# Kernel tuning notes

Measured on AMD Instinct MI355X. Metric: run time of the kernel, lower is better.

The kernel has to match this reference:

```python
import jax, jax.numpy as jnp
import numpy as np

N, E, IN, HID, H, C = 10000, 320000, 64, 64, 4, 64
HC = H * C  # 256


def setup_inputs() -> dict:
    key = jax.random.key(0)
    ks = jax.random.split(key, 40)
    ki = iter(range(40))
    def nrm(shape, scale=0.05):
        return jax.random.normal(ks[next(ki)], shape, dtype=jnp.float32) * scale
    inp = {
        "x": jax.random.normal(ks[next(ki)], (N, IN), dtype=jnp.float32),
        "edge_index": jax.random.randint(ks[next(ki)], (2, E), 0, N, dtype=jnp.int64),
        "lin_w": nrm((IN, HID)), "lin_b": nrm((HID,)),
    }
    dims_in = [HID, HC, HC]
    for i, di in enumerate(dims_in):
        inp[f"gat_w{i}"] = nrm((di, HC))
        inp[f"att_src{i}"] = nrm((H, C))
        inp[f"att_dst{i}"] = nrm((H, C))
        inp[f"gat_b{i}"] = nrm((HC,))
        inp[f"ln_g{i}"] = jnp.ones((HC,), jnp.float32)
        inp[f"ln_b{i}"] = jnp.zeros((HC,), jnp.float32)
    inp["ffn_w1"] = nrm((HC, 2 * HID)); inp["ffn_b1"] = nrm((2 * HID,))
    inp["ffn_w2"] = nrm((2 * HID, 64)); inp["ffn_b2"] = nrm((64,))
    return inp


def _layernorm(x, g, b, eps=1e-5):
    m = jnp.mean(x, -1, keepdims=True)
    v = jnp.var(x, -1, keepdims=True)
    return (x - m) * jax.lax.rsqrt(v + eps) * g + b


def _gat(x, src, dst, w, a_src, a_dst, b):
    # PyG GATConv: per-head linear, additive attention, segment softmax over dst
    xl = (x @ w).reshape(-1, H, C)              # [N,H,C]
    e = jax.nn.leaky_relu(jnp.sum(xl * a_src, -1)[src]
                          + jnp.sum(xl * a_dst, -1)[dst], 0.2)  # [E,H]
    emax = jax.ops.segment_max(e, dst, num_segments=N)
    ex = jnp.exp(e - emax[dst])
    alpha = ex / jax.ops.segment_sum(ex, dst, num_segments=N)[dst]
    out = jax.ops.segment_sum(xl[src] * alpha[:, :, None], dst, num_segments=N)
    return out.reshape(-1, HC) + b


def reference(x, edge_index, lin_w, lin_b,
              gat_w0, att_src0, att_dst0, gat_b0, ln_g0, ln_b0,
              gat_w1, att_src1, att_dst1, gat_b1, ln_g1, ln_b1,
              gat_w2, att_src2, att_dst2, gat_b2, ln_g2, ln_b2,
              ffn_w1, ffn_b1, ffn_w2, ffn_b2):
    loops = jnp.arange(N, dtype=edge_index.dtype)
    src = jnp.concatenate([edge_index[0], loops])  # add_self_loops=True
    dst = jnp.concatenate([edge_index[1], loops])
    h = jax.nn.relu(x @ lin_w + lin_b)
    layers = [(gat_w0, att_src0, att_dst0, gat_b0, ln_g0, ln_b0),
              (gat_w1, att_src1, att_dst1, gat_b1, ln_g1, ln_b1),
              (gat_w2, att_src2, att_dst2, gat_b2, ln_g2, ln_b2)]
    for (w, a_s, a_d, b, g, lb) in layers:
        residual = h
        h = jax.nn.elu(_gat(h, src, dst, w, a_s, a_d, b))
        if residual.shape[-1] != h.shape[-1]:
            residual = jnp.pad(residual, ((0, 0), (0, h.shape[-1] - residual.shape[-1])))
        h = _layernorm(h + residual, g, lb)  # dropout is identity in eval mode
    h = jax.nn.relu(h @ ffn_w1 + ffn_b1)
    return h @ ffn_w2 + ffn_b2
```

## Files before the change

### kernel.cpp

```cpp
#include <hip/hip_runtime.h>

#define N_NODES 10000
#define N_EDGES 320000
#define EL (N_EDGES + N_NODES)
#define HC 256
#define CAP 96

using bf16x8 = __attribute__((ext_vector_type(8))) short;
using f32x4  = __attribute__((ext_vector_type(4))) float;

__device__ __forceinline__ float bf2f(unsigned short u) {
  union { unsigned int i; float f; } v; v.i = ((unsigned int)u) << 16; return v.f;
}
__device__ __forceinline__ unsigned short f2bf(float f) {
  union { float f; unsigned int i; } v; v.f = f;
  unsigned int r = (v.i + 0x7FFFu + ((v.i >> 16) & 1u)) >> 16;
  return (unsigned short)r;
}


__device__ __forceinline__ void convw_body(const float* __restrict__ w,
                                           unsigned short* __restrict__ bt,
                                           int K, int idx) {
  int half = K >> 1;
  if (idx >= 256 * half) return;
  int col = idx / half;
  int k2 = (idx % half) * 2;
  ushort2 o;
  o.x = f2bf(w[(size_t)k2 * 256 + col]);
  o.y = f2bf(w[(size_t)(k2 + 1) * 256 + col]);
  *(ushort2*)(bt + (size_t)col * K + k2) = o;
}

__global__ __launch_bounds__(256) void prep_kernel(
    int* __restrict__ cnt,
    const float* __restrict__ w0, unsigned short* __restrict__ bt0,
    const float* __restrict__ w1, unsigned short* __restrict__ bt1,
    const float* __restrict__ w2, unsigned short* __restrict__ bt2) {
  int b = blockIdx.x, tid = threadIdx.x;
  if (b < 40) {
    int i = b * 256 + tid;
    if (i < N_NODES) cnt[i] = 0;
  } else if (b < 72) {
    convw_body(w0, bt0, 64, (b - 40) * 256 + tid);
  } else if (b < 200) {
    convw_body(w1, bt1, 256, (b - 72) * 256 + tid);
  } else {
    convw_body(w2, bt2, 256, (b - 200) * 256 + tid);
  }
}


__global__ __launch_bounds__(256) void scatter_lin_kernel(
    const int* __restrict__ edges, int* __restrict__ cnt, int* __restrict__ slots,
    const float* __restrict__ A, const float* __restrict__ B,
    const float* __restrict__ bias, float* __restrict__ C) {
  int tid = threadIdx.x;
  if (blockIdx.x < 1290) {
    int e = blockIdx.x * 256 + tid;
    if (e >= EL) return;
    int s, d;
    if (e < N_EDGES) { s = edges[e]; d = edges[N_EDGES + e]; }
    else { s = d = e - N_EDGES; }
    int pos = atomicAdd(&cnt[d], 1);
    slots[d * CAP + pos] = s;
    return;
  }
  __shared__ float As[16][36];
  __shared__ float Bs[32][64];
  int row0 = (blockIdx.x - 1290) * 16;
  int g = tid >> 6, lane = tid & 63;
  float acc[4];
#pragma unroll
  for (int r = 0; r < 4; ++r) acc[r] = 0.f;
  for (int k0 = 0; k0 < 64; k0 += 32) {
    if (tid < 128) {
      int r = tid >> 3;
      int kc = (tid & 7) << 2;
      *(float4*)&As[r][kc] = *(const float4*)(A + (size_t)(row0 + r) * 64 + k0 + kc);
    }
    {
#pragma unroll
      for (int i = 0; i < 2; ++i) {
        int fidx = (i * 256 + tid) * 4;
        int kk = fidx >> 6;
        int cc = fidx & 63;
        *(float4*)&Bs[kk][cc] = *(const float4*)(B + (size_t)(k0 + kk) * 64 + cc);
      }
    }
    __syncthreads();
#pragma unroll
    for (int kk = 0; kk < 32; kk += 4) {
      float a4[4][4];
#pragma unroll
      for (int rr = 0; rr < 4; ++rr) {
        float4 t = *(const float4*)&As[g * 4 + rr][kk];
        a4[rr][0] = t.x; a4[rr][1] = t.y; a4[rr][2] = t.z; a4[rr][3] = t.w;
      }
#pragma unroll
      for (int u = 0; u < 4; ++u) {
        float b = Bs[kk + u][lane];
#pragma unroll
        for (int rr = 0; rr < 4; ++rr) acc[rr] = fmaf(a4[rr][u], b, acc[rr]);
      }
    }
    __syncthreads();
  }
#pragma unroll
  for (int rr = 0; rr < 4; ++rr) {
    int row = row0 + g * 4 + rr;
    C[(size_t)row * 64 + lane] = fmaxf(acc[rr] + bias[lane], 0.f);
  }
}


template <int K>
__global__ __launch_bounds__(256) void gemm_attn_mfma(
    const float* __restrict__ A, const unsigned short* __restrict__ Bt,
    unsigned short* __restrict__ Cb,
    const float* __restrict__ att_src, const float* __restrict__ att_dst,
    float* __restrict__ asrc_out, float* __restrict__ adst_out) {
  __shared__ __align__(16) unsigned short Asw[16 * 64];
  __shared__ __align__(16) unsigned short Bsw[256 * 64];
  int tid = threadIdx.x;
  int wave = tid >> 6, lane = tid & 63;
  int r = lane & 15, g = lane >> 4;
  int row0 = blockIdx.x * 16;

  f32x4 acc[4];
#pragma unroll
  for (int i = 0; i < 4; ++i) acc[i] = {0.f, 0.f, 0.f, 0.f};

  for (int k0 = 0; k0 < K; k0 += 64) {
    {
      int ar = tid >> 4;
      int kc = (tid & 15) << 2;
      float4 av = *(const float4*)(A + (size_t)(row0 + ar) * K + k0 + kc);
      ushort4 o;
      o.x = f2bf(av.x); o.y = f2bf(av.y); o.z = f2bf(av.z); o.w = f2bf(av.w);
      *(ushort4*)((char*)Asw + ((ar * 128 + kc * 2) ^ ((ar & 7) << 4))) = o;
    }
#pragma unroll
    for (int i = 0; i < 8; ++i) {
      int idx = i * 256 + tid;
      int col = idx >> 3;
      int kc8 = idx & 7;
      uint4 v = *(const uint4*)(Bt + (size_t)col * K + k0 + kc8 * 8);
      *(uint4*)((char*)Bsw + ((col * 128 + kc8 * 16) ^ ((col & 7) << 4))) = v;
    }
    __syncthreads();
#pragma unroll
    for (int chunk = 0; chunk < 2; ++chunk) {
      bf16x8 af = *(const bf16x8*)((char*)Asw +
                    ((r * 128 + chunk * 64 + g * 16) ^ ((r & 7) << 4)));
#pragma unroll
      for (int i = 0; i < 4; ++i) {
        int col = (wave * 4 + i) * 16 + r;
        bf16x8 bfr = *(const bf16x8*)((char*)Bsw +
                       ((col * 128 + chunk * 64 + g * 16) ^ ((col & 7) << 4)));
        acc[i] = __builtin_amdgcn_mfma_f32_16x16x32_bf16(af, bfr, acc[i], 0, 0, 0);
      }
    }
    __syncthreads();
  }

  float asv[4], adv[4];
#pragma unroll
  for (int i = 0; i < 4; ++i) {
    int col = (wave * 4 + i) * 16 + r;
    asv[i] = att_src[col];
    adv[i] = att_dst[col];
  }
#pragma unroll
  for (int j = 0; j < 4; ++j) {
    float ps = acc[0][j] * asv[0] + acc[1][j] * asv[1] + acc[2][j] * asv[2] + acc[3][j] * asv[3];
    float pd = acc[0][j] * adv[0] + acc[1][j] * adv[1] + acc[2][j] * adv[2] + acc[3][j] * adv[3];
#pragma unroll
    for (int m = 8; m >= 1; m >>= 1) {
      ps += __shfl_xor(ps, m);
      pd += __shfl_xor(pd, m);
    }
    if (r == 0) {
      int row = row0 + g * 4 + j;
      asrc_out[row * 4 + wave] = ps;
      adst_out[row * 4 + wave] = pd;
    }
  }

#pragma unroll
  for (int i = 0; i < 4; ++i) {
    int col = (wave * 4 + i) * 16 + r;
#pragma unroll
    for (int j = 0; j < 4; ++j) {
      int row = row0 + g * 4 + j;
      Cb[(size_t)row * 256 + col] = f2bf(acc[i][j]);
    }
  }
}


template <int MODE>
__global__ __launch_bounds__(256) void agg_kernel(
    const int* __restrict__ cnt, const int* __restrict__ slots,
    const float* __restrict__ asrc, const float* __restrict__ adst,
    const unsigned short* __restrict__ xb, const float* __restrict__ bias,
    const float* __restrict__ resid, const float* __restrict__ ln_g,
    const float* __restrict__ ln_b, float* __restrict__ hout) {
  int w = threadIdx.x >> 6, lane = threadIdx.x & 63;
  int n = blockIdx.x * 4 + w;
  int lh = lane & 31;
  int half = lane >> 5;
  int h = lh >> 3;
  int ch8 = lh << 3;
  float ad = adst[n * 4 + h];

  int i0 = n * CAP;
  int deg = cnt[n];
  int len0 = (deg + 1) >> 1;
  int beg = i0 + (half ? len0 : 0);
  int end = i0 + (half ? deg : len0);
  int last = end - 1;

  float a0 = 0.f, a1 = 0.f, a2 = 0.f, a3 = 0.f, a4 = 0.f, a5 = 0.f, a6 = 0.f, a7 = 0.f;
  float wsum = 0.f;

  int sA[4];
#pragma unroll
  for (int j = 0; j < 4; ++j) sA[j] = slots[min(beg + j, last)];
  float ca[4]; uint4 cx[4];
#pragma unroll
  for (int j = 0; j < 4; ++j) {
    ca[j] = asrc[sA[j] * 4 + h];
    cx[j] = *(const uint4*)(xb + (size_t)sA[j] * HC + ch8);
  }
#pragma unroll
  for (int j = 0; j < 4; ++j) sA[j] = slots[min(beg + 4 + j, last)];

  for (int base = beg; base < end; base += 4) {
    float na[4]; uint4 nx[4];
#pragma unroll
    for (int j = 0; j < 4; ++j) {
      na[j] = asrc[sA[j] * 4 + h];
      nx[j] = *(const uint4*)(xb + (size_t)sA[j] * HC + ch8);
    }
#pragma unroll
    for (int j = 0; j < 4; ++j) sA[j] = slots[min(base + 8 + j, last)];
#pragma unroll
    for (int j = 0; j < 4; ++j) {
      float e = ca[j] + ad;
      e = e > 0.f ? e : 0.2f * e;
      float wg = __expf(e);
      wg = (base + j < end) ? wg : 0.f;
      wsum += wg;
      a0 = fmaf(wg, bf2f((unsigned short)(cx[j].x & 0xffff)), a0);
      a1 = fmaf(wg, bf2f((unsigned short)(cx[j].x >> 16)), a1);
      a2 = fmaf(wg, bf2f((unsigned short)(cx[j].y & 0xffff)), a2);
      a3 = fmaf(wg, bf2f((unsigned short)(cx[j].y >> 16)), a3);
      a4 = fmaf(wg, bf2f((unsigned short)(cx[j].z & 0xffff)), a4);
      a5 = fmaf(wg, bf2f((unsigned short)(cx[j].z >> 16)), a5);
      a6 = fmaf(wg, bf2f((unsigned short)(cx[j].w & 0xffff)), a6);
      a7 = fmaf(wg, bf2f((unsigned short)(cx[j].w >> 16)), a7);
    }
#pragma unroll
    for (int j = 0; j < 4; ++j) { ca[j] = na[j]; cx[j] = nx[j]; }
  }

  a0 += __shfl_xor(a0, 32); a1 += __shfl_xor(a1, 32);
  a2 += __shfl_xor(a2, 32); a3 += __shfl_xor(a3, 32);
  a4 += __shfl_xor(a4, 32); a5 += __shfl_xor(a5, 32);
  a6 += __shfl_xor(a6, 32); a7 += __shfl_xor(a7, 32);
  wsum += __shfl_xor(wsum, 32);

  int cb = ch8 + half * 4;
  float v0 = half ? a4 : a0;
  float v1 = half ? a5 : a1;
  float v2 = half ? a6 : a2;
  float v3 = half ? a7 : a3;

  float rw = 1.f / wsum;
  float4 b4 = *(const float4*)(bias + cb);
  v0 = fmaf(v0, rw, b4.x);
  v1 = fmaf(v1, rw, b4.y);
  v2 = fmaf(v2, rw, b4.z);
  v3 = fmaf(v3, rw, b4.w);
  v0 = v0 > 0.f ? v0 : __expf(v0) - 1.f;
  v1 = v1 > 0.f ? v1 : __expf(v1) - 1.f;
  v2 = v2 > 0.f ? v2 : __expf(v2) - 1.f;
  v3 = v3 > 0.f ? v3 : __expf(v3) - 1.f;

  if constexpr (MODE == 0) {
    if (cb < 64) {
      float4 r = *(const float4*)(resid + (size_t)n * 64 + cb);
      v0 += r.x; v1 += r.y; v2 += r.z; v3 += r.w;
    }
  } else {
    float4 r = *(const float4*)(resid + (size_t)n * HC + cb);
    v0 += r.x; v1 += r.y; v2 += r.z; v3 += r.w;
  }

  float s1 = v0 + v1 + v2 + v3;
  float s2 = v0 * v0 + v1 * v1 + v2 * v2 + v3 * v3;
#pragma unroll
  for (int m = 32; m >= 1; m >>= 1) {
    s1 += __shfl_xor(s1, m);
    s2 += __shfl_xor(s2, m);
  }
  float mean = s1 * (1.f / 256.f);
  float var = s2 * (1.f / 256.f) - mean * mean;
  float inv = rsqrtf(var + 1e-5f);

  float4 g4 = *(const float4*)(ln_g + cb);
  float4 lb4 = *(const float4*)(ln_b + cb);
  float4 o;
  o.x = (v0 - mean) * inv * g4.x + lb4.x;
  o.y = (v1 - mean) * inv * g4.y + lb4.y;
  o.z = (v2 - mean) * inv * g4.z + lb4.z;
  o.w = (v3 - mean) * inv * g4.w + lb4.w;
  *(float4*)(hout + (size_t)n * HC + cb) = o;
}


__global__ __launch_bounds__(256) void ffn_kernel(const float* __restrict__ A,
                                                  const float* __restrict__ w1,
                                                  const float* __restrict__ b1,
                                                  const float* __restrict__ w2,
                                                  const float* __restrict__ b2,
                                                  float* __restrict__ out) {
  __shared__ float As[16][36];
  __shared__ float Bs[32][128];
  __shared__ float Ms[16][132];
  int tid = threadIdx.x;
  int row0 = blockIdx.x * 16;
  int g = tid >> 6, lane = tid & 63;

  {
    int colBase = lane * 2;
    float acc[4][2];
#pragma unroll
    for (int r = 0; r < 4; ++r) { acc[r][0] = 0.f; acc[r][1] = 0.f; }
    for (int k0 = 0; k0 < 256; k0 += 32) {
      if (tid < 128) {
        int r = tid >> 3;
        int kc = (tid & 7) << 2;
        *(float4*)&As[r][kc] = *(const float4*)(A + (size_t)(row0 + r) * 256 + k0 + kc);
      }
#pragma unroll
      for (int i = 0; i < 4; ++i) {
        int fidx = (i * 256 + tid) * 4;
        int kk = fidx >> 7;
        int cc = fidx & 127;
        *(float4*)&Bs[kk][cc] = *(const float4*)(w1 + (size_t)(k0 + kk) * 128 + cc);
      }
      __syncthreads();
#pragma unroll
      for (int kk = 0; kk < 32; kk += 4) {
        float a4[4][4];
#pragma unroll
        for (int rr = 0; rr < 4; ++rr) {
          float4 t = *(const float4*)&As[g * 4 + rr][kk];
          a4[rr][0] = t.x; a4[rr][1] = t.y; a4[rr][2] = t.z; a4[rr][3] = t.w;
        }
#pragma unroll
        for (int u = 0; u < 4; ++u) {
          float2 b = *(const float2*)&Bs[kk + u][colBase];
#pragma unroll
          for (int rr = 0; rr < 4; ++rr) {
            acc[rr][0] = fmaf(a4[rr][u], b.x, acc[rr][0]);
            acc[rr][1] = fmaf(a4[rr][u], b.y, acc[rr][1]);
          }
        }
      }
      __syncthreads();
    }
    float bb0 = b1[colBase], bb1 = b1[colBase + 1];
#pragma unroll
    for (int rr = 0; rr < 4; ++rr) {
      Ms[g * 4 + rr][colBase]     = fmaxf(acc[rr][0] + bb0, 0.f);
      Ms[g * 4 + rr][colBase + 1] = fmaxf(acc[rr][1] + bb1, 0.f);
    }
  }
  __syncthreads();

  {
    float acc[4];
#pragma unroll
    for (int r = 0; r < 4; ++r) acc[r] = 0.f;
    for (int k0 = 0; k0 < 128; k0 += 32) {
#pragma unroll
      for (int i = 0; i < 2; ++i) {
        int fidx = (i * 256 + tid) * 4;
        int kk = fidx >> 6;
        int cc = fidx & 63;
        *(float4*)&Bs[kk][cc] = *(const float4*)(w2 + (size_t)(k0 + kk) * 64 + cc);
      }
      __syncthreads();
#pragma unroll
      for (int kk = 0; kk < 32; ++kk) {
        float b = Bs[kk][lane];
#pragma unroll
        for (int rr = 0; rr < 4; ++rr)
          acc[rr] = fmaf(Ms[g * 4 + rr][k0 + kk], b, acc[rr]);
      }
      __syncthreads();
    }
    float bb = b2[lane];
#pragma unroll
    for (int rr = 0; rr < 4; ++rr) {
      int row = row0 + g * 4 + rr;
      out[(size_t)row * 64 + lane] = acc[rr] + bb;
    }
  }
}


extern "C" void kernel_launch(void* const* d_in, const int* in_sizes, int n_in,
                              void* d_out, int out_size, void* d_ws, size_t ws_size,
                              hipStream_t stream) {
  (void)in_sizes; (void)n_in; (void)out_size; (void)ws_size;
  const float* x      = (const float*)d_in[0];
  const int*   edges  = (const int*)d_in[1];
  const float* lin_w  = (const float*)d_in[2];
  const float* lin_b  = (const float*)d_in[3];
  const float* gat_w[3] = {(const float*)d_in[4], (const float*)d_in[10], (const float*)d_in[16]};
  const float* att_s[3] = {(const float*)d_in[5], (const float*)d_in[11], (const float*)d_in[17]};
  const float* att_d[3] = {(const float*)d_in[6], (const float*)d_in[12], (const float*)d_in[18]};
  const float* gat_b[3] = {(const float*)d_in[7], (const float*)d_in[13], (const float*)d_in[19]};
  const float* ln_g[3]  = {(const float*)d_in[8], (const float*)d_in[14], (const float*)d_in[20]};
  const float* ln_b[3]  = {(const float*)d_in[9], (const float*)d_in[15], (const float*)d_in[21]};
  const float* ffn_w1 = (const float*)d_in[22];
  const float* ffn_b1 = (const float*)d_in[23];
  const float* ffn_w2 = (const float*)d_in[24];
  const float* ffn_b2 = (const float*)d_in[25];

  char* p = (char*)d_ws;
  auto alloc = [&](size_t bytes) {
    char* q = p;
    p += (bytes + 255) & ~(size_t)255;
    return q;
  };
  int* cnt   = (int*)alloc(N_NODES * 4);
  int* slots = (int*)alloc((size_t)N_NODES * CAP * 4);
  float* h0  = (float*)alloc((size_t)N_NODES * 64 * 4);
  float* hA  = (float*)alloc((size_t)N_NODES * HC * 4);
  float* hB  = (float*)alloc((size_t)N_NODES * HC * 4);
  unsigned short* xb = (unsigned short*)alloc((size_t)N_NODES * HC * 2);
  float* as4 = (float*)alloc((size_t)N_NODES * 16);
  float* ad4 = (float*)alloc((size_t)N_NODES * 16);
  unsigned short* bt0 = (unsigned short*)alloc(256 * 64 * 2);
  unsigned short* bt1 = (unsigned short*)alloc(256 * 256 * 2);
  unsigned short* bt2 = (unsigned short*)alloc(256 * 256 * 2);

  const int gblk = N_NODES / 16;
  const int nblk = N_NODES / 4;

  prep_kernel<<<328, 256, 0, stream>>>(cnt, gat_w[0], bt0, gat_w[1], bt1, gat_w[2], bt2);
  scatter_lin_kernel<<<1290 + 625, 256, 0, stream>>>(edges, cnt, slots, x, lin_w, lin_b, h0);

  gemm_attn_mfma<64><<<gblk, 256, 0, stream>>>(h0, bt0, xb, att_s[0], att_d[0], as4, ad4);
  agg_kernel<0><<<nblk, 256, 0, stream>>>(cnt, slots, as4, ad4, xb, gat_b[0], h0,
                                          ln_g[0], ln_b[0], hA);
  gemm_attn_mfma<256><<<gblk, 256, 0, stream>>>(hA, bt1, xb, att_s[1], att_d[1], as4, ad4);
  agg_kernel<1><<<nblk, 256, 0, stream>>>(cnt, slots, as4, ad4, xb, gat_b[1], hA,
                                          ln_g[1], ln_b[1], hB);
  gemm_attn_mfma<256><<<gblk, 256, 0, stream>>>(hB, bt2, xb, att_s[2], att_d[2], as4, ad4);
  agg_kernel<1><<<nblk, 256, 0, stream>>>(cnt, slots, as4, ad4, xb, gat_b[2], hB,
                                          ln_g[2], ln_b[2], hA);

  ffn_kernel<<<gblk, 256, 0, stream>>>(hA, ffn_w1, ffn_b1, ffn_w2, ffn_b2, (float*)d_out);
}
```

Before: 153.9 us.

## Fuse all stages into one cooperative persistent kernel with grid syncs

Replaces the nine separate kernel launches with a single cooperative persistent kernel. Each former kernel becomes a grid-stride phase, and the phases are separated by grid.sync(). The aim is to remove launch overhead and the drain/refill gaps between kernels. In exchange, the shared-memory union limits occupancy, each grid barrier has its own cost, and the grid size is set from an occupancy query that assumes 256 CUs.

```diff
diff --git a/kernel.cpp b/kernel.cpp
--- a/kernel.cpp
+++ b/kernel.cpp
@@ -1,4 +1,7 @@
 #include <hip/hip_runtime.h>
+#include <hip/hip_cooperative_groups.h>
+
+namespace cg = cooperative_groups;
 
 #define N_NODES 10000
 #define N_EDGES 320000
@@ -18,12 +21,25 @@
   return (unsigned short)r;
 }
 
+struct MegaParams {
+  const int* edges;
+  const float* x; const float* lin_w; const float* lin_b;
+  const float* gw0; const float* as0; const float* ad0; const float* gb0; const float* lg0; const float* lb0;
+  const float* gw1; const float* as1; const float* ad1; const float* gb1; const float* lg1; const float* lb1;
+  const float* gw2; const float* as2; const float* ad2; const float* gb2; const float* lg2; const float* lb2;
+  const float* fw1; const float* fb1; const float* fw2; const float* fb2;
+  int* cnt; int* slots;
+  float* h0; float* hA; float* hB;
+  unsigned short* xb;
+  float* as4; float* ad4;
+  unsigned short* bt0; unsigned short* bt1; unsigned short* bt2;
+  float* out;
+};
 
 __device__ __forceinline__ void convw_body(const float* __restrict__ w,
                                            unsigned short* __restrict__ bt,
                                            int K, int idx) {
   int half = K >> 1;
-  if (idx >= 256 * half) return;
   int col = idx / half;
   int k2 = (idx % half) * 2;
   ushort2 o;
@@ -32,61 +48,25 @@
   *(ushort2*)(bt + (size_t)col * K + k2) = o;
 }
 
-__global__ __launch_bounds__(256) void prep_kernel(
-    int* __restrict__ cnt,
-    const float* __restrict__ w0, unsigned short* __restrict__ bt0,
-    const float* __restrict__ w1, unsigned short* __restrict__ bt1,
-    const float* __restrict__ w2, unsigned short* __restrict__ bt2) {
-  int b = blockIdx.x, tid = threadIdx.x;
-  if (b < 40) {
-    int i = b * 256 + tid;
-    if (i < N_NODES) cnt[i] = 0;
-  } else if (b < 72) {
-    convw_body(w0, bt0, 64, (b - 40) * 256 + tid);
-  } else if (b < 200) {
-    convw_body(w1, bt1, 256, (b - 72) * 256 + tid);
-  } else {
-    convw_body(w2, bt2, 256, (b - 200) * 256 + tid);
-  }
-}
-
-
-__global__ __launch_bounds__(256) void scatter_lin_kernel(
-    const int* __restrict__ edges, int* __restrict__ cnt, int* __restrict__ slots,
-    const float* __restrict__ A, const float* __restrict__ B,
-    const float* __restrict__ bias, float* __restrict__ C) {
-  int tid = threadIdx.x;
-  if (blockIdx.x < 1290) {
-    int e = blockIdx.x * 256 + tid;
-    if (e >= EL) return;
-    int s, d;
-    if (e < N_EDGES) { s = edges[e]; d = edges[N_EDGES + e]; }
-    else { s = d = e - N_EDGES; }
-    int pos = atomicAdd(&cnt[d], 1);
-    slots[d * CAP + pos] = s;
-    return;
-  }
-  __shared__ float As[16][36];
-  __shared__ float Bs[32][64];
-  int row0 = (blockIdx.x - 1290) * 16;
+__device__ void lin_tile(char* smem, int t, const float* __restrict__ A,
+                         const float* __restrict__ B, const float* __restrict__ bias,
+                         float* __restrict__ C, int tid) {
+  float (*As)[36] = (float(*)[36])smem;
+  float (*Bs)[64] = (float(*)[64])(smem + 2304);
+  int row0 = t * 16;
   int g = tid >> 6, lane = tid & 63;
-  float acc[4];
-#pragma unroll
-  for (int r = 0; r < 4; ++r) acc[r] = 0.f;
+  float acc[4] = {0.f, 0.f, 0.f, 0.f};
   for (int k0 = 0; k0 < 64; k0 += 32) {
     if (tid < 128) {
       int r = tid >> 3;
       int kc = (tid & 7) << 2;
       *(float4*)&As[r][kc] = *(const float4*)(A + (size_t)(row0 + r) * 64 + k0 + kc);
     }
-    {
-#pragma unroll
-      for (int i = 0; i < 2; ++i) {
-        int fidx = (i * 256 + tid) * 4;
-        int kk = fidx >> 6;
-        int cc = fidx & 63;
-        *(float4*)&Bs[kk][cc] = *(const float4*)(B + (size_t)(k0 + kk) * 64 + cc);
-      }
+#pragma unroll
+    for (int i = 0; i < 2; ++i) {
+      int fidx = (i * 256 + tid) * 4;
+      *(float4*)&Bs[fidx >> 6][fidx & 63] =
+          *(const float4*)(B + (size_t)(k0 + (fidx >> 6)) * 64 + (fidx & 63));
     }
     __syncthreads();
 #pragma unroll
@@ -94,8 +74,8 @@
       float a4[4][4];
 #pragma unroll
       for (int rr = 0; rr < 4; ++rr) {
-        float4 t = *(const float4*)&As[g * 4 + rr][kk];
-        a4[rr][0] = t.x; a4[rr][1] = t.y; a4[rr][2] = t.z; a4[rr][3] = t.w;
+        float4 tv = *(const float4*)&As[g * 4 + rr][kk];
+        a4[rr][0] = tv.x; a4[rr][1] = tv.y; a4[rr][2] = tv.z; a4[rr][3] = tv.w;
       }
 #pragma unroll
       for (int u = 0; u < 4; ++u) {
@@ -113,19 +93,17 @@
   }
 }
 
-
 template <int K>
-__global__ __launch_bounds__(256) void gemm_attn_mfma(
-    const float* __restrict__ A, const unsigned short* __restrict__ Bt,
-    unsigned short* __restrict__ Cb,
-    const float* __restrict__ att_src, const float* __restrict__ att_dst,
-    float* __restrict__ asrc_out, float* __restrict__ adst_out) {
-  __shared__ __align__(16) unsigned short Asw[16 * 64];
-  __shared__ __align__(16) unsigned short Bsw[256 * 64];
-  int tid = threadIdx.x;
+__device__ void mfma_tile(char* smem, int t, const float* __restrict__ A,
+                          const unsigned short* __restrict__ Bt,
+                          unsigned short* __restrict__ Cb,
+                          const float* __restrict__ att_src, const float* __restrict__ att_dst,
+                          float* __restrict__ asrc_out, float* __restrict__ adst_out, int tid) {
+  char* Asw = smem;
+  char* Bsw = smem + 2048;
   int wave = tid >> 6, lane = tid & 63;
   int r = lane & 15, g = lane >> 4;
-  int row0 = blockIdx.x * 16;
+  int row0 = t * 16;
 
   f32x4 acc[4];
 #pragma unroll
@@ -138,7 +116,7 @@
       float4 av = *(const float4*)(A + (size_t)(row0 + ar) * K + k0 + kc);
       ushort4 o;
       o.x = f2bf(av.x); o.y = f2bf(av.y); o.z = f2bf(av.z); o.w = f2bf(av.w);
-      *(ushort4*)((char*)Asw + ((ar * 128 + kc * 2) ^ ((ar & 7) << 4))) = o;
+      *(ushort4*)(Asw + ((ar * 128 + kc * 2) ^ ((ar & 7) << 4))) = o;
     }
 #pragma unroll
     for (int i = 0; i < 8; ++i) {
@@ -146,18 +124,16 @@
       int col = idx >> 3;
       int kc8 = idx & 7;
       uint4 v = *(const uint4*)(Bt + (size_t)col * K + k0 + kc8 * 8);
-      *(uint4*)((char*)Bsw + ((col * 128 + kc8 * 16) ^ ((col & 7) << 4))) = v;
+      *(uint4*)(Bsw + ((col * 128 + kc8 * 16) ^ ((col & 7) << 4))) = v;
     }
     __syncthreads();
 #pragma unroll
     for (int chunk = 0; chunk < 2; ++chunk) {
-      bf16x8 af = *(const bf16x8*)((char*)Asw +
-                    ((r * 128 + chunk * 64 + g * 16) ^ ((r & 7) << 4)));
+      bf16x8 af = *(const bf16x8*)(Asw + ((r * 128 + chunk * 64 + g * 16) ^ ((r & 7) << 4)));
 #pragma unroll
       for (int i = 0; i < 4; ++i) {
         int col = (wave * 4 + i) * 16 + r;
-        bf16x8 bfr = *(const bf16x8*)((char*)Bsw +
-                       ((col * 128 + chunk * 64 + g * 16) ^ ((col & 7) << 4)));
+        bf16x8 bfr = *(const bf16x8*)(Bsw + ((col * 128 + chunk * 64 + g * 16) ^ ((col & 7) << 4)));
         acc[i] = __builtin_amdgcn_mfma_f32_16x16x32_bf16(af, bfr, acc[i], 0, 0, 0);
       }
     }
@@ -198,16 +174,14 @@
   }
 }
 
-
 template <int MODE>
-__global__ __launch_bounds__(256) void agg_kernel(
-    const int* __restrict__ cnt, const int* __restrict__ slots,
-    const float* __restrict__ asrc, const float* __restrict__ adst,
-    const unsigned short* __restrict__ xb, const float* __restrict__ bias,
-    const float* __restrict__ resid, const float* __restrict__ ln_g,
-    const float* __restrict__ ln_b, float* __restrict__ hout) {
-  int w = threadIdx.x >> 6, lane = threadIdx.x & 63;
-  int n = blockIdx.x * 4 + w;
+__device__ void agg_group(int gidx, const int* __restrict__ cnt, const int* __restrict__ slots,
+                          const float* __restrict__ asrc, const float* __restrict__ adst,
+                          const unsigned short* __restrict__ xb, const float* __restrict__ bias,
+                          const float* __restrict__ resid, const float* __restrict__ ln_g,
+                          const float* __restrict__ ln_b, float* __restrict__ hout, int tid) {
+  int w = tid >> 6, lane = tid & 63;
+  int n = gidx * 4 + w;
   int lh = lane & 31;
   int half = lane >> 5;
   int h = lh >> 3;
@@ -319,18 +293,14 @@
   *(float4*)(hout + (size_t)n * HC + cb) = o;
 }
 
-
-__global__ __launch_bounds__(256) void ffn_kernel(const float* __restrict__ A,
-                                                  const float* __restrict__ w1,
-                                                  const float* __restrict__ b1,
-                                                  const float* __restrict__ w2,
-                                                  const float* __restrict__ b2,
-                                                  float* __restrict__ out) {
-  __shared__ float As[16][36];
-  __shared__ float Bs[32][128];
-  __shared__ float Ms[16][132];
-  int tid = threadIdx.x;
-  int row0 = blockIdx.x * 16;
+__device__ void ffn_tile(char* smem, int t, const float* __restrict__ A,
+                         const float* __restrict__ w1, const float* __restrict__ b1,
+                         const float* __restrict__ w2, const float* __restrict__ b2,
+                         float* __restrict__ out, int tid) {
+  float (*As)[36] = (float(*)[36])smem;
+  float (*Bs)[128] = (float(*)[128])(smem + 2304);
+  float (*Ms)[132] = (float(*)[132])(smem + 18688);
+  int row0 = t * 16;
   int g = tid >> 6, lane = tid & 63;
 
   {
@@ -347,9 +317,8 @@
 #pragma unroll
       for (int i = 0; i < 4; ++i) {
         int fidx = (i * 256 + tid) * 4;
-        int kk = fidx >> 7;
-        int cc = fidx & 127;
-        *(float4*)&Bs[kk][cc] = *(const float4*)(w1 + (size_t)(k0 + kk) * 128 + cc);
+        *(float4*)&Bs[fidx >> 7][fidx & 127] =
+            *(const float4*)(w1 + (size_t)(k0 + (fidx >> 7)) * 128 + (fidx & 127));
       }
       __syncthreads();
 #pragma unroll
@@ -357,8 +326,8 @@
         float a4[4][4];
 #pragma unroll
         for (int rr = 0; rr < 4; ++rr) {
-          float4 t = *(const float4*)&As[g * 4 + rr][kk];
-          a4[rr][0] = t.x; a4[rr][1] = t.y; a4[rr][2] = t.z; a4[rr][3] = t.w;
+          float4 tv = *(const float4*)&As[g * 4 + rr][kk];
+          a4[rr][0] = tv.x; a4[rr][1] = tv.y; a4[rr][2] = tv.z; a4[rr][3] = tv.w;
         }
 #pragma unroll
         for (int u = 0; u < 4; ++u) {
@@ -382,16 +351,13 @@
   __syncthreads();
 
   {
-    float acc[4];
-#pragma unroll
-    for (int r = 0; r < 4; ++r) acc[r] = 0.f;
+    float acc[4] = {0.f, 0.f, 0.f, 0.f};
     for (int k0 = 0; k0 < 128; k0 += 32) {
 #pragma unroll
       for (int i = 0; i < 2; ++i) {
         int fidx = (i * 256 + tid) * 4;
-        int kk = fidx >> 6;
-        int cc = fidx & 63;
-        *(float4*)&Bs[kk][cc] = *(const float4*)(w2 + (size_t)(k0 + kk) * 64 + cc);
+        *(float4*)&Bs[fidx >> 6][fidx & 63] =
+            *(const float4*)(w2 + (size_t)(k0 + (fidx >> 6)) * 64 + (fidx & 63));
       }
       __syncthreads();
 #pragma unroll
@@ -410,6 +376,56 @@
       out[(size_t)row * 64 + lane] = acc[rr] + bb;
     }
   }
+}
+
+
+__global__ __launch_bounds__(256) void mega_kernel(MegaParams p) {
+  __shared__ __align__(16) char smem[34816];
+  cg::grid_group grid = cg::this_grid();
+  int tid = threadIdx.x;
+  int gtid = blockIdx.x * 256 + tid;
+  int stride = gridDim.x * 256;
+
+  for (int i = gtid; i < N_NODES; i += stride) p.cnt[i] = 0;
+  for (int i = gtid; i < 256 * 32; i += stride) convw_body(p.gw0, p.bt0, 64, i);
+  for (int i = gtid; i < 256 * 128; i += stride) convw_body(p.gw1, p.bt1, 256, i);
+  for (int i = gtid; i < 256 * 128; i += stride) convw_body(p.gw2, p.bt2, 256, i);
+  grid.sync();
+
+  for (int t = blockIdx.x; t < 625; t += gridDim.x)
+    lin_tile(smem, t, p.x, p.lin_w, p.lin_b, p.h0, tid);
+  for (int e = gtid; e < EL; e += stride) {
+    int s, d;
+    if (e < N_EDGES) { s = p.edges[e]; d = p.edges[N_EDGES + e]; }
+    else { s = d = e - N_EDGES; }
+    int pos = atomicAdd(&p.cnt[d], 1);
+    p.slots[d * CAP + pos] = s;
+  }
+  grid.sync();
+
+  for (int t = blockIdx.x; t < 625; t += gridDim.x)
+    mfma_tile<64>(smem, t, p.h0, p.bt0, p.xb, p.as0, p.ad0, p.as4, p.ad4, tid);
+  grid.sync();
+  for (int g2 = blockIdx.x; g2 < 2500; g2 += gridDim.x)
+    agg_group<0>(g2, p.cnt, p.slots, p.as4, p.ad4, p.xb, p.gb0, p.h0, p.lg0, p.lb0, p.hA, tid);
+  grid.sync();
+
+  for (int t = blockIdx.x; t < 625; t += gridDim.x)
+    mfma_tile<256>(smem, t, p.hA, p.bt1, p.xb, p.as1, p.ad1, p.as4, p.ad4, tid);
+  grid.sync();
+  for (int g2 = blockIdx.x; g2 < 2500; g2 += gridDim.x)
+    agg_group<1>(g2, p.cnt, p.slots, p.as4, p.ad4, p.xb, p.gb1, p.hA, p.lg1, p.lb1, p.hB, tid);
+  grid.sync();
+
+  for (int t = blockIdx.x; t < 625; t += gridDim.x)
+    mfma_tile<256>(smem, t, p.hB, p.bt2, p.xb, p.as2, p.ad2, p.as4, p.ad4, tid);
+  grid.sync();
+  for (int g2 = blockIdx.x; g2 < 2500; g2 += gridDim.x)
+    agg_group<1>(g2, p.cnt, p.slots, p.as4, p.ad4, p.xb, p.gb2, p.hB, p.lg2, p.lb2, p.hA, tid);
+  grid.sync();
+
+  for (int t = blockIdx.x; t < 625; t += gridDim.x)
+    ffn_tile(smem, t, p.hA, p.fw1, p.fb1, p.fw2, p.fb2, p.out, tid);
 }
 
 
@@ -417,25 +433,11 @@
                               void* d_out, int out_size, void* d_ws, size_t ws_size,
                               hipStream_t stream) {
   (void)in_sizes; (void)n_in; (void)out_size; (void)ws_size;
-  const float* x      = (const float*)d_in[0];
-  const int*   edges  = (const int*)d_in[1];
-  const float* lin_w  = (const float*)d_in[2];
-  const float* lin_b  = (const float*)d_in[3];
-  const float* gat_w[3] = {(const float*)d_in[4], (const float*)d_in[10], (const float*)d_in[16]};
-  const float* att_s[3] = {(const float*)d_in[5], (const float*)d_in[11], (const float*)d_in[17]};
-  const float* att_d[3] = {(const float*)d_in[6], (const float*)d_in[12], (const float*)d_in[18]};
-  const float* gat_b[3] = {(const float*)d_in[7], (const float*)d_in[13], (const float*)d_in[19]};
-  const float* ln_g[3]  = {(const float*)d_in[8], (const float*)d_in[14], (const float*)d_in[20]};
-  const float* ln_b[3]  = {(const float*)d_in[9], (const float*)d_in[15], (const float*)d_in[21]};
-  const float* ffn_w1 = (const float*)d_in[22];
-  const float* ffn_b1 = (const float*)d_in[23];
-  const float* ffn_w2 = (const float*)d_in[24];
-  const float* ffn_b2 = (const float*)d_in[25];
-
-  char* p = (char*)d_ws;
+
+  char* wp = (char*)d_ws;
   auto alloc = [&](size_t bytes) {
-    char* q = p;
-    p += (bytes + 255) & ~(size_t)255;
+    char* q = wp;
+    wp += (bytes + 255) & ~(size_t)255;
     return q;
   };
   int* cnt   = (int*)alloc(N_NODES * 4);
@@ -450,21 +452,28 @@
   unsigned short* bt1 = (unsigned short*)alloc(256 * 256 * 2);
   unsigned short* bt2 = (unsigned short*)alloc(256 * 256 * 2);
 
-  const int gblk = N_NODES / 16;
-  const int nblk = N_NODES / 4;
-
-  prep_kernel<<<328, 256, 0, stream>>>(cnt, gat_w[0], bt0, gat_w[1], bt1, gat_w[2], bt2);
-  scatter_lin_kernel<<<1290 + 625, 256, 0, stream>>>(edges, cnt, slots, x, lin_w, lin_b, h0);
-
-  gemm_attn_mfma<64><<<gblk, 256, 0, stream>>>(h0, bt0, xb, att_s[0], att_d[0], as4, ad4);
-  agg_kernel<0><<<nblk, 256, 0, stream>>>(cnt, slots, as4, ad4, xb, gat_b[0], h0,
-                                          ln_g[0], ln_b[0], hA);
-  gemm_attn_mfma<256><<<gblk, 256, 0, stream>>>(hA, bt1, xb, att_s[1], att_d[1], as4, ad4);
-  agg_kernel<1><<<nblk, 256, 0, stream>>>(cnt, slots, as4, ad4, xb, gat_b[1], hA,
-                                          ln_g[1], ln_b[1], hB);
-  gemm_attn_mfma<256><<<gblk, 256, 0, stream>>>(hB, bt2, xb, att_s[2], att_d[2], as4, ad4);
-  agg_kernel<1><<<nblk, 256, 0, stream>>>(cnt, slots, as4, ad4, xb, gat_b[2], hB,
-                                          ln_g[2], ln_b[2], hA);
-
-  ffn_kernel<<<gblk, 256, 0, stream>>>(hA, ffn_w1, ffn_b1, ffn_w2, ffn_b2, (float*)d_out);
-}
+  MegaParams p;
+  p.edges = (const int*)d_in[1];
+  p.x = (const float*)d_in[0]; p.lin_w = (const float*)d_in[2]; p.lin_b = (const float*)d_in[3];
+  p.gw0 = (const float*)d_in[4];  p.as0 = (const float*)d_in[5];  p.ad0 = (const float*)d_in[6];
+  p.gb0 = (const float*)d_in[7];  p.lg0 = (const float*)d_in[8];  p.lb0 = (const float*)d_in[9];
+  p.gw1 = (const float*)d_in[10]; p.as1 = (const float*)d_in[11]; p.ad1 = (const float*)d_in[12];
+  p.gb1 = (const float*)d_in[13]; p.lg1 = (const float*)d_in[14]; p.lb1 = (const float*)d_in[15];
+  p.gw2 = (const float*)d_in[16]; p.as2 = (const float*)d_in[17]; p.ad2 = (const float*)d_in[18];
+  p.gb2 = (const float*)d_in[19]; p.lg2 = (const float*)d_in[20]; p.lb2 = (const float*)d_in[21];
+  p.fw1 = (const float*)d_in[22]; p.fb1 = (const float*)d_in[23];
+  p.fw2 = (const float*)d_in[24]; p.fb2 = (const float*)d_in[25];
+  p.cnt = cnt; p.slots = slots; p.h0 = h0; p.hA = hA; p.hB = hB;
+  p.xb = xb; p.as4 = as4; p.ad4 = ad4; p.bt0 = bt0; p.bt1 = bt1; p.bt2 = bt2;
+  p.out = (float*)d_out;
+
+  int nb = 0;
+  hipOccupancyMaxActiveBlocksPerMultiprocessor(&nb, mega_kernel, 256, 0);
+  if (nb < 1) nb = 1;
+  if (nb > 8) nb = 8;
+  int grid = nb * 256;
+  if (grid > 2500) grid = 2500;
+
+  void* kargs[] = {(void*)&p};
+  hipLaunchCooperativeKernel((void*)mega_kernel, dim3(grid), dim3(256), kargs, 0, stream);
+}
```

Result: slower. 551.3 us (+258.3%).

## Store hidden activations in bf16 and fold weight conversion into scatter kernel

Applied to the files above, without the earlier changes.

Intermediate node features (h0, hA, hB) are now stored as bf16 instead of fp32. The GEMM loads them directly without converting, while the aggregation residual path and the FFN widen them on load. This halves the activation traffic between kernels and removes the per-load f32-to-bf16 conversion in the GEMM. The weight bf16 transposition moves from the prep kernel into extra blocks of the scatter/linear kernel, leaving prep to only zero the counters. The trade-off is lower precision in the residual and LayerNorm outputs.

```diff
diff --git a/kernel.cpp b/kernel.cpp
--- a/kernel.cpp
+++ b/kernel.cpp
@@ -19,11 +19,16 @@
 }
 
 
+__global__ __launch_bounds__(256) void prep_kernel(int* __restrict__ cnt) {
+  int i = blockIdx.x * 256 + threadIdx.x;
+  if (i < N_NODES) cnt[i] = 0;
+}
+
+
 __device__ __forceinline__ void convw_body(const float* __restrict__ w,
                                            unsigned short* __restrict__ bt,
                                            int K, int idx) {
   int half = K >> 1;
-  if (idx >= 256 * half) return;
   int col = idx / half;
   int k2 = (idx % half) * 2;
   ushort2 o;
@@ -32,32 +37,17 @@
   *(ushort2*)(bt + (size_t)col * K + k2) = o;
 }
 
-__global__ __launch_bounds__(256) void prep_kernel(
-    int* __restrict__ cnt,
+__global__ __launch_bounds__(256) void scatter_lin_kernel(
+    const int* __restrict__ edges, int* __restrict__ cnt, int* __restrict__ slots,
+    const float* __restrict__ A, const float* __restrict__ B,
+    const float* __restrict__ bias, unsigned short* __restrict__ C,
     const float* __restrict__ w0, unsigned short* __restrict__ bt0,
     const float* __restrict__ w1, unsigned short* __restrict__ bt1,
     const float* __restrict__ w2, unsigned short* __restrict__ bt2) {
-  int b = blockIdx.x, tid = threadIdx.x;
-  if (b < 40) {
-    int i = b * 256 + tid;
-    if (i < N_NODES) cnt[i] = 0;
-  } else if (b < 72) {
-    convw_body(w0, bt0, 64, (b - 40) * 256 + tid);
-  } else if (b < 200) {
-    convw_body(w1, bt1, 256, (b - 72) * 256 + tid);
-  } else {
-    convw_body(w2, bt2, 256, (b - 200) * 256 + tid);
-  }
-}
-
-
-__global__ __launch_bounds__(256) void scatter_lin_kernel(
-    const int* __restrict__ edges, int* __restrict__ cnt, int* __restrict__ slots,
-    const float* __restrict__ A, const float* __restrict__ B,
-    const float* __restrict__ bias, float* __restrict__ C) {
   int tid = threadIdx.x;
-  if (blockIdx.x < 1290) {
-    int e = blockIdx.x * 256 + tid;
+  int b = blockIdx.x;
+  if (b < 1290) {
+    int e = b * 256 + tid;
     if (e >= EL) return;
     int s, d;
     if (e < N_EDGES) { s = edges[e]; d = edges[N_EDGES + e]; }
@@ -66,27 +56,28 @@
     slots[d * CAP + pos] = s;
     return;
   }
+  if (b >= 1915) {
+    if (b < 1947) convw_body(w0, bt0, 64, (b - 1915) * 256 + tid);
+    else if (b < 2075) convw_body(w1, bt1, 256, (b - 1947) * 256 + tid);
+    else convw_body(w2, bt2, 256, (b - 2075) * 256 + tid);
+    return;
+  }
   __shared__ float As[16][36];
   __shared__ float Bs[32][64];
-  int row0 = (blockIdx.x - 1290) * 16;
+  int row0 = (b - 1290) * 16;
   int g = tid >> 6, lane = tid & 63;
-  float acc[4];
-#pragma unroll
-  for (int r = 0; r < 4; ++r) acc[r] = 0.f;
+  float acc[4] = {0.f, 0.f, 0.f, 0.f};
   for (int k0 = 0; k0 < 64; k0 += 32) {
     if (tid < 128) {
       int r = tid >> 3;
       int kc = (tid & 7) << 2;
       *(float4*)&As[r][kc] = *(const float4*)(A + (size_t)(row0 + r) * 64 + k0 + kc);
     }
-    {
-#pragma unroll
-      for (int i = 0; i < 2; ++i) {
-        int fidx = (i * 256 + tid) * 4;
-        int kk = fidx >> 6;
-        int cc = fidx & 63;
-        *(float4*)&Bs[kk][cc] = *(const float4*)(B + (size_t)(k0 + kk) * 64 + cc);
-      }
+#pragma unroll
+    for (int i = 0; i < 2; ++i) {
+      int fidx = (i * 256 + tid) * 4;
+      *(float4*)&Bs[fidx >> 6][fidx & 63] =
+          *(const float4*)(B + (size_t)(k0 + (fidx >> 6)) * 64 + (fidx & 63));
     }
     __syncthreads();
 #pragma unroll
@@ -99,9 +90,9 @@
       }
 #pragma unroll
       for (int u = 0; u < 4; ++u) {
-        float b = Bs[kk + u][lane];
-#pragma unroll
-        for (int rr = 0; rr < 4; ++rr) acc[rr] = fmaf(a4[rr][u], b, acc[rr]);
+        float bb = Bs[kk + u][lane];
+#pragma unroll
+        for (int rr = 0; rr < 4; ++rr) acc[rr] = fmaf(a4[rr][u], bb, acc[rr]);
       }
     }
     __syncthreads();
@@ -109,14 +100,14 @@
 #pragma unroll
   for (int rr = 0; rr < 4; ++rr) {
     int row = row0 + g * 4 + rr;
-    C[(size_t)row * 64 + lane] = fmaxf(acc[rr] + bias[lane], 0.f);
+    C[(size_t)row * 64 + lane] = f2bf(fmaxf(acc[rr] + bias[lane], 0.f));
   }
 }
 
 
 template <int K>
 __global__ __launch_bounds__(256) void gemm_attn_mfma(
-    const float* __restrict__ A, const unsigned short* __restrict__ Bt,
+    const unsigned short* __restrict__ A, const unsigned short* __restrict__ Bt,
     unsigned short* __restrict__ Cb,
     const float* __restrict__ att_src, const float* __restrict__ att_dst,
     float* __restrict__ asrc_out, float* __restrict__ adst_out) {
@@ -135,10 +126,8 @@
     {
       int ar = tid >> 4;
       int kc = (tid & 15) << 2;
-      float4 av = *(const float4*)(A + (size_t)(row0 + ar) * K + k0 + kc);
-      ushort4 o;
-      o.x = f2bf(av.x); o.y = f2bf(av.y); o.z = f2bf(av.z); o.w = f2bf(av.w);
-      *(ushort4*)((char*)Asw + ((ar * 128 + kc * 2) ^ ((ar & 7) << 4))) = o;
+      ushort4 av = *(const ushort4*)(A + (size_t)(row0 + ar) * K + k0 + kc);
+      *(ushort4*)((char*)Asw + ((ar * 128 + kc * 2) ^ ((ar & 7) << 4))) = av;
     }
 #pragma unroll
     for (int i = 0; i < 8; ++i) {
@@ -204,8 +193,8 @@
     const int* __restrict__ cnt, const int* __restrict__ slots,
     const float* __restrict__ asrc, const float* __restrict__ adst,
     const unsigned short* __restrict__ xb, const float* __restrict__ bias,
-    const float* __restrict__ resid, const float* __restrict__ ln_g,
-    const float* __restrict__ ln_b, float* __restrict__ hout) {
+    const unsigned short* __restrict__ resid, const float* __restrict__ ln_g,
+    const float* __restrict__ ln_b, unsigned short* __restrict__ hout) {
   int w = threadIdx.x >> 6, lane = threadIdx.x & 63;
   int n = blockIdx.x * 4 + w;
   int lh = lane & 31;
@@ -290,12 +279,12 @@
 
   if constexpr (MODE == 0) {
     if (cb < 64) {
-      float4 r = *(const float4*)(resid + (size_t)n * 64 + cb);
-      v0 += r.x; v1 += r.y; v2 += r.z; v3 += r.w;
+      ushort4 r4 = *(const ushort4*)(resid + (size_t)n * 64 + cb);
+      v0 += bf2f(r4.x); v1 += bf2f(r4.y); v2 += bf2f(r4.z); v3 += bf2f(r4.w);
     }
   } else {
-    float4 r = *(const float4*)(resid + (size_t)n * HC + cb);
-    v0 += r.x; v1 += r.y; v2 += r.z; v3 += r.w;
+    ushort4 r4 = *(const ushort4*)(resid + (size_t)n * HC + cb);
+    v0 += bf2f(r4.x); v1 += bf2f(r4.y); v2 += bf2f(r4.z); v3 += bf2f(r4.w);
   }
 
   float s1 = v0 + v1 + v2 + v3;
@@ -311,16 +300,16 @@
 
   float4 g4 = *(const float4*)(ln_g + cb);
   float4 lb4 = *(const float4*)(ln_b + cb);
-  float4 o;
-  o.x = (v0 - mean) * inv * g4.x + lb4.x;
-  o.y = (v1 - mean) * inv * g4.y + lb4.y;
-  o.z = (v2 - mean) * inv * g4.z + lb4.z;
-  o.w = (v3 - mean) * inv * g4.w + lb4.w;
-  *(float4*)(hout + (size_t)n * HC + cb) = o;
-}
-
-
-__global__ __launch_bounds__(256) void ffn_kernel(const float* __restrict__ A,
+  ushort4 o;
+  o.x = f2bf((v0 - mean) * inv * g4.x + lb4.x);
+  o.y = f2bf((v1 - mean) * inv * g4.y + lb4.y);
+  o.z = f2bf((v2 - mean) * inv * g4.z + lb4.z);
+  o.w = f2bf((v3 - mean) * inv * g4.w + lb4.w);
+  *(ushort4*)(hout + (size_t)n * HC + cb) = o;
+}
+
+
+__global__ __launch_bounds__(256) void ffn_kernel(const unsigned short* __restrict__ A,
                                                   const float* __restrict__ w1,
                                                   const float* __restrict__ b1,
                                                   const float* __restrict__ w2,
@@ -342,14 +331,17 @@
       if (tid < 128) {
         int r = tid >> 3;
         int kc = (tid & 7) << 2;
-        *(float4*)&As[r][kc] = *(const float4*)(A + (size_t)(row0 + r) * 256 + k0 + kc);
+        ushort4 av = *(const ushort4*)(A + (size_t)(row0 + r) * 256 + k0 + kc);
+        As[r][kc]     = bf2f(av.x);
+        As[r][kc + 1] = bf2f(av.y);
+        As[r][kc + 2] = bf2f(av.z);
+        As[r][kc + 3] = bf2f(av.w);
       }
 #pragma unroll
       for (int i = 0; i < 4; ++i) {
         int fidx = (i * 256 + tid) * 4;
-        int kk = fidx >> 7;
-        int cc = fidx & 127;
-        *(float4*)&Bs[kk][cc] = *(const float4*)(w1 + (size_t)(k0 + kk) * 128 + cc);
+        *(float4*)&Bs[fidx >> 7][fidx & 127] =
+            *(const float4*)(w1 + (size_t)(k0 + (fidx >> 7)) * 128 + (fidx & 127));
       }
       __syncthreads();
 #pragma unroll
@@ -357,8 +349,8 @@
         float a4[4][4];
 #pragma unroll
         for (int rr = 0; rr < 4; ++rr) {
-          float4 t = *(const float4*)&As[g * 4 + rr][kk];
-          a4[rr][0] = t.x; a4[rr][1] = t.y; a4[rr][2] = t.z; a4[rr][3] = t.w;
+          float4 tv = *(const float4*)&As[g * 4 + rr][kk];
+          a4[rr][0] = tv.x; a4[rr][1] = tv.y; a4[rr][2] = tv.z; a4[rr][3] = tv.w;
         }
 #pragma unroll
         for (int u = 0; u < 4; ++u) {
@@ -382,16 +374,13 @@
   __syncthreads();
 
   {
-    float acc[4];
-#pragma unroll
-    for (int r = 0; r < 4; ++r) acc[r] = 0.f;
+    float acc[4] = {0.f, 0.f, 0.f, 0.f};
     for (int k0 = 0; k0 < 128; k0 += 32) {
 #pragma unroll
       for (int i = 0; i < 2; ++i) {
         int fidx = (i * 256 + tid) * 4;
-        int kk = fidx >> 6;
-        int cc = fidx & 63;
-        *(float4*)&Bs[kk][cc] = *(const float4*)(w2 + (size_t)(k0 + kk) * 64 + cc);
+        *(float4*)&Bs[fidx >> 6][fidx & 63] =
+            *(const float4*)(w2 + (size_t)(k0 + (fidx >> 6)) * 64 + (fidx & 63));
       }
       __syncthreads();
 #pragma unroll
@@ -440,9 +429,9 @@
   };
   int* cnt   = (int*)alloc(N_NODES * 4);
   int* slots = (int*)alloc((size_t)N_NODES * CAP * 4);
-  float* h0  = (float*)alloc((size_t)N_NODES * 64 * 4);
-  float* hA  = (float*)alloc((size_t)N_NODES * HC * 4);
-  float* hB  = (float*)alloc((size_t)N_NODES * HC * 4);
+  unsigned short* h0 = (unsigned short*)alloc((size_t)N_NODES * 64 * 2);
+  unsigned short* hA = (unsigned short*)alloc((size_t)N_NODES * HC * 2);
+  unsigned short* hB = (unsigned short*)alloc((size_t)N_NODES * HC * 2);
   unsigned short* xb = (unsigned short*)alloc((size_t)N_NODES * HC * 2);
   float* as4 = (float*)alloc((size_t)N_NODES * 16);
   float* ad4 = (float*)alloc((size_t)N_NODES * 16);
@@ -453,8 +442,9 @@
   const int gblk = N_NODES / 16;
   const int nblk = N_NODES / 4;
 
-  prep_kernel<<<328, 256, 0, stream>>>(cnt, gat_w[0], bt0, gat_w[1], bt1, gat_w[2], bt2);
-  scatter_lin_kernel<<<1290 + 625, 256, 0, stream>>>(edges, cnt, slots, x, lin_w, lin_b, h0);
+  prep_kernel<<<40, 256, 0, stream>>>(cnt);
+  scatter_lin_kernel<<<2203, 256, 0, stream>>>(edges, cnt, slots, x, lin_w, lin_b, h0,
+                                               gat_w[0], bt0, gat_w[1], bt1, gat_w[2], bt2);
 
   gemm_attn_mfma<64><<<gblk, 256, 0, stream>>>(h0, bt0, xb, att_s[0], att_d[0], as4, ad4);
   agg_kernel<0><<<nblk, 256, 0, stream>>>(cnt, slots, as4, ad4, xb, gat_b[0], h0,
```

Result: no change. 156.4 us (+1.6%).
